# Kernel tuning notes

Measured on AMD Instinct MI355X. Metric: run time of the kernel, lower is better.

Reference implementation:

```python
import jax, jax.numpy as jnp
import numpy as np


def setup_inputs() -> dict:
    key = jax.random.key(0)
    ks = jax.random.split(key, 5)
    B, H, W, C, R = 4, 64, 64, 256, 32
    x = jax.random.normal(ks[0], (B, H, W, C), dtype=jnp.float32)
    # 1x1 conv kernels stored as [C_in, C_out] matrices (equivalent math)
    w_f = jax.random.normal(ks[1], (C, R), dtype=jnp.float32) * (1.0 / np.sqrt(C))
    w_g = jax.random.normal(ks[2], (C, R), dtype=jnp.float32) * (1.0 / np.sqrt(C))
    w_h = jax.random.normal(ks[3], (C, R), dtype=jnp.float32) * (1.0 / np.sqrt(C))
    w_v = jax.random.normal(ks[4], (R, C), dtype=jnp.float32) * (1.0 / np.sqrt(R))
    gamma = jnp.zeros((1,), dtype=jnp.float32)
    return {"x": x, "w_f": w_f, "w_g": w_g, "w_h": w_h, "w_v": w_v, "gamma": gamma}


def reference(x, w_f, w_g, w_h, w_v, gamma):
    B, H, W, C = x.shape
    N = H * W
    xt = x.reshape(B, N, C)                       # flatten spatial tokens
    f = jnp.einsum('bnc,cr->bnr', xt, w_f)        # 1x1 conv == token-wise matmul
    g = jnp.einsum('bnc,cr->bnr', xt, w_g)
    h = jnp.einsum('bnc,cr->bnr', xt, w_h)
    scores = jnp.einsum('bnr,bmr->bnm', f, g)     # [B, N, N]
    # NOTE: original softmaxes over axis=1 (the query/row axis), not axis=-1
    attn = jax.nn.softmax(scores, axis=1)
    y = jnp.einsum('bnm,bmr->bnr', attn, h)       # [B, N, R]
    y = jnp.einsum('bnr,rc->bnc', y, w_v)         # output 1x1 conv
    y = y.reshape(B, H, W, C)
    return gamma * y + x
```

## Files before the change

kernel.cpp:

```cpp
#include <hip/hip_runtime.h>


#define BB 4
#define NN 4096
#define CC 256
#define RR 32
#define CSEG 4
#define PSEG 4
#define MP 40
#define LOG2E 1.44269504088896340736f

typedef short short8 __attribute__((ext_vector_type(8)));
typedef float floatx4 __attribute__((ext_vector_type(4)));

#define MFMA16 __builtin_amdgcn_mfma_f32_16x16x32_bf16

static __device__ __forceinline__ unsigned short f2bf(float f) {
  union { float f; unsigned u; } v; v.f = f;
  const unsigned r = v.u + 0x7fffu + ((v.u >> 16) & 1u);
  return (unsigned short)(r >> 16);
}
static __device__ __forceinline__ unsigned bfpack(float lo, float hi) {
  return __builtin_amdgcn_perm(__float_as_uint(hi), __float_as_uint(lo), 0x07060302u);
}

__global__ __launch_bounds__(256) void k_prep(
    const float* __restrict__ wf, const float* __restrict__ wg,
    const float* __restrict__ wh, const float* __restrict__ wv,
    unsigned short* __restrict__ wfrag, unsigned short* __restrict__ wvfrag) {
  const int idx = blockIdx.x * 256 + threadIdx.x;
  const int lane = (idx >> 3) & 63;
  const int j = idx & 7;
  const int col = lane & 15, q = lane >> 4;
  if (idx < 24576) {
    const int mat = idx >> 13;
    const int fid = (idx >> 9) & 15;
    const int kc = fid >> 1, nt = fid & 1;
    const float* w = (mat == 0) ? wf : ((mat == 1) ? wg : wh);
    wfrag[idx] = f2bf(w[(kc * 32 + q * 8 + j) * RR + nt * 16 + col]);
  } else {
    const int r = idx - 24576;
    const int t = (r >> 9) & 15;
    wvfrag[r] = f2bf(wv[(q * 8 + j) * CC + t * 16 + col]);
  }
}

__global__ __launch_bounds__(256) void k_fgh(
    const float* __restrict__ x, const unsigned short* __restrict__ wfrag,
    unsigned short* __restrict__ f16, unsigned short* __restrict__ g16,
    unsigned short* __restrict__ hT16) {
  const int tid = threadIdx.x, lane = tid & 63, wave = tid >> 6;
  const int col = lane & 15, q = lane >> 4;
  const int t0 = blockIdx.x * 64 + wave * 16;
  short8 af[8];
  const float* xr = x + (long)(t0 + col) * CC + q * 8;
#pragma unroll
  for (int kc = 0; kc < 8; ++kc) {
    float tmp[8];
    *(float4*)(tmp) = *(const float4*)(xr + kc * 32);
    *(float4*)(tmp + 4) = *(const float4*)(xr + kc * 32 + 4);
    short8 o;
#pragma unroll
    for (int j = 0; j < 8; ++j) o[j] = (short)f2bf(tmp[j]);
    af[kc] = o;
  }
  const floatx4 zero = {0.f, 0.f, 0.f, 0.f};
  floatx4 acc[3][2];
#pragma unroll
  for (int m = 0; m < 3; ++m) { acc[m][0] = zero; acc[m][1] = zero; }
  const short8* wfr = (const short8*)wfrag;
#pragma unroll
  for (int kc = 0; kc < 8; ++kc) {
#pragma unroll
    for (int mat = 0; mat < 3; ++mat) {
#pragma unroll
      for (int nt = 0; nt < 2; ++nt) {
        const short8 bf = wfr[(mat * 16 + kc * 2 + nt) * 64 + lane];
        acc[mat][nt] = MFMA16(af[kc], bf, acc[mat][nt], 0, 0, 0);
      }
    }
  }
  const int b = t0 >> 12;
#pragma unroll
  for (int nt = 0; nt < 2; ++nt) {
#pragma unroll
    for (int r = 0; r < 4; ++r) {
      const int tok = t0 + q * 4 + r;
      const int n = nt * 16 + col;
      f16[(long)tok * RR + n] = f2bf(acc[0][nt][r] * LOG2E);
      g16[(long)tok * RR + n] = f2bf(acc[1][nt][r]);
      hT16[((long)b * RR + n) * NN + (tok & (NN - 1))] = f2bf(acc[2][nt][r]);
    }
  }
}

__global__ __launch_bounds__(256) void k_colsum(
    const unsigned short* __restrict__ f16, const unsigned short* __restrict__ g16,
    float* __restrict__ psum) {
  const int tid = threadIdx.x, lane = tid & 63, wave = tid >> 6;
  const int col = lane & 15, q = lane >> 4;
  const int mblk = blockIdx.x & 31;
  const int b = (blockIdx.x >> 5) & 3;
  const int seg = blockIdx.x >> 7;
  const int m0 = mblk * 128 + wave * 32;
  const short8 bg1 = *(const short8*)(g16 + ((long)(b * NN + m0 + col)) * RR + q * 8);
  const short8 bg2 = *(const short8*)(g16 + ((long)(b * NN + m0 + 16 + col)) * RR + q * 8);
  const floatx4 zero = {0.f, 0.f, 0.f, 0.f};
  float s1 = 0.f, s2 = 0.f;
  const unsigned short* fb = f16 + ((long)b * NN + seg * (NN / CSEG)) * RR;
#pragma unroll 4
  for (int n = 0; n < NN / CSEG; n += 16) {
    const short8 af = *(const short8*)(fb + (long)(n + col) * RR + q * 8);
    const floatx4 d1 = MFMA16(af, bg1, zero, 0, 0, 0);
    const floatx4 d2 = MFMA16(af, bg2, zero, 0, 0, 0);
    s1 += __builtin_amdgcn_exp2f(d1[0]) + __builtin_amdgcn_exp2f(d1[1]) +
          __builtin_amdgcn_exp2f(d1[2]) + __builtin_amdgcn_exp2f(d1[3]);
    s2 += __builtin_amdgcn_exp2f(d2[0]) + __builtin_amdgcn_exp2f(d2[1]) +
          __builtin_amdgcn_exp2f(d2[2]) + __builtin_amdgcn_exp2f(d2[3]);
  }
  s1 += __shfl_xor(s1, 16); s1 += __shfl_xor(s1, 32);
  s2 += __shfl_xor(s2, 16); s2 += __shfl_xor(s2, 32);
  if (lane < 16) {
    psum[(long)seg * (BB * NN) + b * NN + m0 + lane] = s1;
    psum[(long)seg * (BB * NN) + b * NN + m0 + 16 + lane] = s2;
  }
}

#define C_ADDR(TN, TM) (((TN) + col) * MP + (TM) + q * 4)
__global__ __launch_bounds__(256) void k_pv(
    const unsigned short* __restrict__ f16, const unsigned short* __restrict__ g16,
    const unsigned short* __restrict__ hT16, const float* __restrict__ psum,
    float* __restrict__ py) {
  __shared__ unsigned short pt_all[4][32 * MP];
  __shared__ float cis[NN / PSEG];
  const int tid = threadIdx.x, lane = tid & 63, wave = tid >> 6;
  const int col = lane & 15, q = lane >> 4;
  const int nblk = blockIdx.x & 31;
  const int b = (blockIdx.x >> 5) & 3;
  const int mseg = blockIdx.x >> 7;
  const int n0 = nblk * 128 + wave * 32;
  const int mbase = mseg * (NN / PSEG);
  for (int i = tid; i < NN / PSEG; i += 256) {
    float s = 0.f;
#pragma unroll
    for (int sg = 0; sg < CSEG; ++sg) s += psum[(long)sg * (BB * NN) + b * NN + mbase + i];
    cis[i] = 1.0f / s;
  }
  __syncthreads();
  const short8 af1 = *(const short8*)(f16 + ((long)(b * NN + n0 + col)) * RR + q * 8);
  const short8 af2 = *(const short8*)(f16 + ((long)(b * NN + n0 + 16 + col)) * RR + q * 8);
  const floatx4 zero = {0.f, 0.f, 0.f, 0.f};
  floatx4 a11 = zero, a12 = zero, a21 = zero, a22 = zero;
  unsigned short* pt = &pt_all[wave][0];
  const unsigned short* gb = g16 + (long)b * NN * RR;
  const unsigned short* hb = hT16 + (long)b * RR * NN;
  for (int mi = 0; mi < NN / PSEG; mi += 32) {
    const int m0 = mbase + mi;
    const short8 bg1 = *(const short8*)(gb + (long)(m0 + col) * RR + q * 8);
    const short8 bg2 = *(const short8*)(gb + (long)(m0 + 16 + col) * RR + q * 8);
    const floatx4 d00 = MFMA16(bg1, af1, zero, 0, 0, 0);
    const floatx4 d01 = MFMA16(bg2, af1, zero, 0, 0, 0);
    const floatx4 d10 = MFMA16(bg1, af2, zero, 0, 0, 0);
    const floatx4 d11 = MFMA16(bg2, af2, zero, 0, 0, 0);
    const float4 cia = *(const float4*)(cis + mi + q * 4);
    const float4 cib = *(const float4*)(cis + mi + 16 + q * 4);
    {
      float w0, w1, w2, w3;
      w0 = __builtin_amdgcn_exp2f(d00[0]) * cia.x; w1 = __builtin_amdgcn_exp2f(d00[1]) * cia.y;
      w2 = __builtin_amdgcn_exp2f(d00[2]) * cia.z; w3 = __builtin_amdgcn_exp2f(d00[3]) * cia.w;
      *(uint2*)(pt + C_ADDR(0, 0)) = make_uint2(bfpack(w0, w1), bfpack(w2, w3));
      w0 = __builtin_amdgcn_exp2f(d01[0]) * cib.x; w1 = __builtin_amdgcn_exp2f(d01[1]) * cib.y;
      w2 = __builtin_amdgcn_exp2f(d01[2]) * cib.z; w3 = __builtin_amdgcn_exp2f(d01[3]) * cib.w;
      *(uint2*)(pt + C_ADDR(0, 16)) = make_uint2(bfpack(w0, w1), bfpack(w2, w3));
      w0 = __builtin_amdgcn_exp2f(d10[0]) * cia.x; w1 = __builtin_amdgcn_exp2f(d10[1]) * cia.y;
      w2 = __builtin_amdgcn_exp2f(d10[2]) * cia.z; w3 = __builtin_amdgcn_exp2f(d10[3]) * cia.w;
      *(uint2*)(pt + C_ADDR(16, 0)) = make_uint2(bfpack(w0, w1), bfpack(w2, w3));
      w0 = __builtin_amdgcn_exp2f(d11[0]) * cib.x; w1 = __builtin_amdgcn_exp2f(d11[1]) * cib.y;
      w2 = __builtin_amdgcn_exp2f(d11[2]) * cib.z; w3 = __builtin_amdgcn_exp2f(d11[3]) * cib.w;
      *(uint2*)(pt + C_ADDR(16, 16)) = make_uint2(bfpack(w0, w1), bfpack(w2, w3));
    }
    const short8 ap1 = *(const short8*)(pt + col * MP + q * 8);
    const short8 ap2 = *(const short8*)(pt + (col + 16) * MP + q * 8);
    const short8 bh1 = *(const short8*)(hb + (long)col * NN + m0 + q * 8);
    const short8 bh2 = *(const short8*)(hb + (long)(col + 16) * NN + m0 + q * 8);
    a11 = MFMA16(ap1, bh1, a11, 0, 0, 0);
    a12 = MFMA16(ap1, bh2, a12, 0, 0, 0);
    a21 = MFMA16(ap2, bh1, a21, 0, 0, 0);
    a22 = MFMA16(ap2, bh2, a22, 0, 0, 0);
  }
  float* yp = py + (long)(mseg * BB + b) * NN * RR;
#pragma unroll
  for (int r = 0; r < 4; ++r) {
    yp[(long)(n0 + q * 4 + r) * RR + col]           = a11[r];
    yp[(long)(n0 + q * 4 + r) * RR + col + 16]      = a12[r];
    yp[(long)(n0 + 16 + q * 4 + r) * RR + col]      = a21[r];
    yp[(long)(n0 + 16 + q * 4 + r) * RR + col + 16] = a22[r];
  }
}

__global__ __launch_bounds__(256) void k_out(
    const float* __restrict__ py, const unsigned short* __restrict__ wvfrag,
    const float* __restrict__ x, const float* __restrict__ gamma,
    float* __restrict__ out) {
  __shared__ float ot[4][16 * 132];
  const int tid = threadIdx.x, lane = tid & 63, wave = tid >> 6;
  const int col = lane & 15, q = lane >> 4;
  const int t0 = blockIdx.x * 64 + wave * 16;
  const int b = t0 >> 12;
  const int tloc = t0 & (NN - 1);
  float s[8] = {0.f, 0.f, 0.f, 0.f, 0.f, 0.f, 0.f, 0.f};
#pragma unroll
  for (int sg = 0; sg < PSEG; ++sg) {
    const float* p = py + ((long)(sg * BB + b) * NN + tloc + col) * RR + q * 8;
    const float4 u0 = *(const float4*)p;
    const float4 u1 = *(const float4*)(p + 4);
    s[0] += u0.x; s[1] += u0.y; s[2] += u0.z; s[3] += u0.w;
    s[4] += u1.x; s[5] += u1.y; s[6] += u1.z; s[7] += u1.w;
  }
  short8 ay;
#pragma unroll
  for (int j = 0; j < 8; ++j) ay[j] = (short)f2bf(s[j]);
  const float gm = gamma[0];
  const floatx4 zero = {0.f, 0.f, 0.f, 0.f};
  const short8* wvf = (const short8*)wvfrag;
  float* pw = &ot[wave][0];
  const int tok = lane >> 2, cg = (lane & 3) * 4;
#pragma unroll
  for (int h = 0; h < 2; ++h) {
#pragma unroll
    for (int t = 0; t < 8; ++t) {
      const short8 bw = wvf[(h * 8 + t) * 64 + lane];
      const floatx4 d = MFMA16(ay, bw, zero, 0, 0, 0);
#pragma unroll
      for (int r = 0; r < 4; ++r) pw[(q * 4 + r) * 132 + t * 16 + col] = d[r];
    }
#pragma unroll
    for (int j = 0; j < 8; ++j) {
      const float4 v = *(const float4*)(pw + tok * 132 + cg + j * 16);
      const long gidx = (long)(t0 + tok) * CC + h * 128 + cg + j * 16;
      const float4 xv = *(const float4*)(x + gidx);
      float4 o;
      o.x = gm * v.x + xv.x; o.y = gm * v.y + xv.y;
      o.z = gm * v.z + xv.z; o.w = gm * v.w + xv.w;
      *(float4*)(out + gidx) = o;
    }
  }
}

extern "C" void kernel_launch(void* const* d_in, const int* in_sizes, int n_in,
                              void* d_out, int out_size, void* d_ws, size_t ws_size,
                              hipStream_t stream) {
  const float* x = (const float*)d_in[0];
  const float* wf = (const float*)d_in[1];
  const float* wg = (const float*)d_in[2];
  const float* wh = (const float*)d_in[3];
  const float* wv = (const float*)d_in[4];
  const float* gamma = (const float*)d_in[5];
  float* out = (float*)d_out;

  unsigned short* wfrag = (unsigned short*)d_ws;
  unsigned short* wvfrag = wfrag + 24576;
  unsigned short* f16 = wvfrag + 8192;
  unsigned short* g16 = f16 + (long)BB * NN * RR;
  unsigned short* hT16 = g16 + (long)BB * NN * RR;
  float* psum = (float*)(hT16 + (long)BB * NN * RR);
  float* py = psum + (long)CSEG * BB * NN;

  k_prep<<<128, 256, 0, stream>>>(wf, wg, wh, wv, wfrag, wvfrag);
  k_fgh<<<BB * NN / 64, 256, 0, stream>>>(x, wfrag, f16, g16, hT16);
  k_colsum<<<CSEG * BB * 32, 256, 0, stream>>>(f16, g16, psum);
  k_pv<<<PSEG * BB * 32, 256, 0, stream>>>(f16, g16, hT16, psum, py);
  k_out<<<BB * NN / 64, 256, 0, stream>>>(py, wvfrag, x, gamma, out);
}
```

Before: 131.7 us.

## Fuse five stage kernels into one cooperative kernel with grid syncs

Replaces the five separate launches (weight prep, f/g/h projection, column sums, PV, output projection) with a single cooperative kernel of 512 blocks that uses grid-wide barriers between stages. The aim is to remove per-launch overhead and inter-kernel gaps. The fgh and output stages now run on only two of four waves per block, with 32 tokens per block, and shared memory is aliased between stages. The cost is four grid barriers and a grid size limited by co-residency (launch bounds of 2 blocks per CU).

```diff
diff --git a/kernel.cpp b/kernel.cpp
--- a/kernel.cpp
+++ b/kernel.cpp
@@ -1,4 +1,7 @@
 #include <hip/hip_runtime.h>
+#include <hip/hip_cooperative_groups.h>
+
+namespace cg = cooperative_groups;
 
 
 #define BB 4
@@ -24,147 +27,143 @@
   return __builtin_amdgcn_perm(__float_as_uint(hi), __float_as_uint(lo), 0x07060302u);
 }
 
-__global__ __launch_bounds__(256) void k_prep(
-    const float* __restrict__ wf, const float* __restrict__ wg,
-    const float* __restrict__ wh, const float* __restrict__ wv,
-    unsigned short* __restrict__ wfrag, unsigned short* __restrict__ wvfrag) {
-  const int idx = blockIdx.x * 256 + threadIdx.x;
-  const int lane = (idx >> 3) & 63;
-  const int j = idx & 7;
-  const int col = lane & 15, q = lane >> 4;
-  if (idx < 24576) {
-    const int mat = idx >> 13;
-    const int fid = (idx >> 9) & 15;
-    const int kc = fid >> 1, nt = fid & 1;
-    const float* w = (mat == 0) ? wf : ((mat == 1) ? wg : wh);
-    wfrag[idx] = f2bf(w[(kc * 32 + q * 8 + j) * RR + nt * 16 + col]);
-  } else {
-    const int r = idx - 24576;
-    const int t = (r >> 9) & 15;
-    wvfrag[r] = f2bf(wv[(q * 8 + j) * CC + t * 16 + col]);
-  }
-}
-
-__global__ __launch_bounds__(256) void k_fgh(
-    const float* __restrict__ x, const unsigned short* __restrict__ wfrag,
+#define C_ADDR(TN, TM) (((TN) + col) * MP + (TM) + q * 4)
+
+__global__ __launch_bounds__(256, 2) void k_all(
+    const float* __restrict__ x, const float* __restrict__ wf,
+    const float* __restrict__ wg, const float* __restrict__ wh,
+    const float* __restrict__ wv, const float* __restrict__ gamma,
+    float* __restrict__ out,
+    unsigned short* __restrict__ wfrag, unsigned short* __restrict__ wvfrag,
     unsigned short* __restrict__ f16, unsigned short* __restrict__ g16,
-    unsigned short* __restrict__ hT16) {
+    unsigned short* __restrict__ hT16, float* __restrict__ psum,
+    float* __restrict__ py) {
+  cg::grid_group gg = cg::this_grid();
+  __shared__ __align__(16) unsigned char smem[16896];
   const int tid = threadIdx.x, lane = tid & 63, wave = tid >> 6;
   const int col = lane & 15, q = lane >> 4;
-  const int t0 = blockIdx.x * 64 + wave * 16;
-  short8 af[8];
-  const float* xr = x + (long)(t0 + col) * CC + q * 8;
-#pragma unroll
-  for (int kc = 0; kc < 8; ++kc) {
-    float tmp[8];
-    *(float4*)(tmp) = *(const float4*)(xr + kc * 32);
-    *(float4*)(tmp + 4) = *(const float4*)(xr + kc * 32 + 4);
-    short8 o;
-#pragma unroll
-    for (int j = 0; j < 8; ++j) o[j] = (short)f2bf(tmp[j]);
-    af[kc] = o;
-  }
+  const int blk = blockIdx.x;
   const floatx4 zero = {0.f, 0.f, 0.f, 0.f};
-  floatx4 acc[3][2];
-#pragma unroll
-  for (int m = 0; m < 3; ++m) { acc[m][0] = zero; acc[m][1] = zero; }
-  const short8* wfr = (const short8*)wfrag;
-#pragma unroll
-  for (int kc = 0; kc < 8; ++kc) {
-#pragma unroll
-    for (int mat = 0; mat < 3; ++mat) {
-#pragma unroll
-      for (int nt = 0; nt < 2; ++nt) {
-        const short8 bf = wfr[(mat * 16 + kc * 2 + nt) * 64 + lane];
-        acc[mat][nt] = MFMA16(af[kc], bf, acc[mat][nt], 0, 0, 0);
-      }
-    }
-  }
-  const int b = t0 >> 12;
-#pragma unroll
-  for (int nt = 0; nt < 2; ++nt) {
-#pragma unroll
-    for (int r = 0; r < 4; ++r) {
-      const int tok = t0 + q * 4 + r;
-      const int n = nt * 16 + col;
-      f16[(long)tok * RR + n] = f2bf(acc[0][nt][r] * LOG2E);
-      g16[(long)tok * RR + n] = f2bf(acc[1][nt][r]);
-      hT16[((long)b * RR + n) * NN + (tok & (NN - 1))] = f2bf(acc[2][nt][r]);
-    }
-  }
-}
-
-__global__ __launch_bounds__(256) void k_colsum(
-    const unsigned short* __restrict__ f16, const unsigned short* __restrict__ g16,
-    float* __restrict__ psum) {
-  const int tid = threadIdx.x, lane = tid & 63, wave = tid >> 6;
-  const int col = lane & 15, q = lane >> 4;
-  const int mblk = blockIdx.x & 31;
-  const int b = (blockIdx.x >> 5) & 3;
-  const int seg = blockIdx.x >> 7;
-  const int m0 = mblk * 128 + wave * 32;
-  const short8 bg1 = *(const short8*)(g16 + ((long)(b * NN + m0 + col)) * RR + q * 8);
-  const short8 bg2 = *(const short8*)(g16 + ((long)(b * NN + m0 + 16 + col)) * RR + q * 8);
-  const floatx4 zero = {0.f, 0.f, 0.f, 0.f};
-  float s1 = 0.f, s2 = 0.f;
-  const unsigned short* fb = f16 + ((long)b * NN + seg * (NN / CSEG)) * RR;
+
+  {
+    const int idx = blk * 256 + tid;
+    if (idx < 24576) {
+      const int mat = idx >> 13;
+      const int fid = (idx >> 9) & 15;
+      const int kc = fid >> 1, nt = fid & 1;
+      const int l2 = (idx >> 3) & 63, j = idx & 7;
+      const int c2 = l2 & 15, q2 = l2 >> 4;
+      const float* w = (mat == 0) ? wf : ((mat == 1) ? wg : wh);
+      wfrag[idx] = f2bf(w[(kc * 32 + q2 * 8 + j) * RR + nt * 16 + c2]);
+    } else if (idx < 32768) {
+      const int r = idx - 24576;
+      const int t = (r >> 9) & 15;
+      const int l2 = (r >> 3) & 63, j = r & 7;
+      const int c2 = l2 & 15, q2 = l2 >> 4;
+      wvfrag[r] = f2bf(wv[(q2 * 8 + j) * CC + t * 16 + c2]);
+    }
+  }
+  gg.sync();
+
+  if (wave < 2) {
+    const int t0 = blk * 32 + wave * 16;
+    short8 af[8];
+    const float* xr = x + (long)(t0 + col) * CC + q * 8;
+#pragma unroll
+    for (int kc = 0; kc < 8; ++kc) {
+      float tmp[8];
+      *(float4*)(tmp) = *(const float4*)(xr + kc * 32);
+      *(float4*)(tmp + 4) = *(const float4*)(xr + kc * 32 + 4);
+      short8 o;
+#pragma unroll
+      for (int j = 0; j < 8; ++j) o[j] = (short)f2bf(tmp[j]);
+      af[kc] = o;
+    }
+    floatx4 acc[3][2];
+#pragma unroll
+    for (int m = 0; m < 3; ++m) { acc[m][0] = zero; acc[m][1] = zero; }
+    const short8* wfr = (const short8*)wfrag;
+#pragma unroll
+    for (int kc = 0; kc < 8; ++kc) {
+#pragma unroll
+      for (int mat = 0; mat < 3; ++mat) {
+#pragma unroll
+        for (int nt = 0; nt < 2; ++nt) {
+          const short8 bf = wfr[(mat * 16 + kc * 2 + nt) * 64 + lane];
+          acc[mat][nt] = MFMA16(af[kc], bf, acc[mat][nt], 0, 0, 0);
+        }
+      }
+    }
+    const int b = t0 >> 12;
+#pragma unroll
+    for (int nt = 0; nt < 2; ++nt) {
+#pragma unroll
+      for (int r = 0; r < 4; ++r) {
+        const int tok = t0 + q * 4 + r;
+        const int n = nt * 16 + col;
+        f16[(long)tok * RR + n] = f2bf(acc[0][nt][r] * LOG2E);
+        g16[(long)tok * RR + n] = f2bf(acc[1][nt][r]);
+        hT16[((long)b * RR + n) * NN + (tok & (NN - 1))] = f2bf(acc[2][nt][r]);
+      }
+    }
+  }
+  gg.sync();
+
+  {
+    const int mblk = blk & 31, b = (blk >> 5) & 3, seg = blk >> 7;
+    const int m0 = mblk * 128 + wave * 32;
+    const short8 bg1 = *(const short8*)(g16 + ((long)(b * NN + m0 + col)) * RR + q * 8);
+    const short8 bg2 = *(const short8*)(g16 + ((long)(b * NN + m0 + 16 + col)) * RR + q * 8);
+    float s1 = 0.f, s2 = 0.f;
+    const unsigned short* fb = f16 + ((long)b * NN + seg * (NN / CSEG)) * RR;
 #pragma unroll 4
-  for (int n = 0; n < NN / CSEG; n += 16) {
-    const short8 af = *(const short8*)(fb + (long)(n + col) * RR + q * 8);
-    const floatx4 d1 = MFMA16(af, bg1, zero, 0, 0, 0);
-    const floatx4 d2 = MFMA16(af, bg2, zero, 0, 0, 0);
-    s1 += __builtin_amdgcn_exp2f(d1[0]) + __builtin_amdgcn_exp2f(d1[1]) +
-          __builtin_amdgcn_exp2f(d1[2]) + __builtin_amdgcn_exp2f(d1[3]);
-    s2 += __builtin_amdgcn_exp2f(d2[0]) + __builtin_amdgcn_exp2f(d2[1]) +
-          __builtin_amdgcn_exp2f(d2[2]) + __builtin_amdgcn_exp2f(d2[3]);
-  }
-  s1 += __shfl_xor(s1, 16); s1 += __shfl_xor(s1, 32);
-  s2 += __shfl_xor(s2, 16); s2 += __shfl_xor(s2, 32);
-  if (lane < 16) {
-    psum[(long)seg * (BB * NN) + b * NN + m0 + lane] = s1;
-    psum[(long)seg * (BB * NN) + b * NN + m0 + 16 + lane] = s2;
-  }
-}
-
-#define C_ADDR(TN, TM) (((TN) + col) * MP + (TM) + q * 4)
-__global__ __launch_bounds__(256) void k_pv(
-    const unsigned short* __restrict__ f16, const unsigned short* __restrict__ g16,
-    const unsigned short* __restrict__ hT16, const float* __restrict__ psum,
-    float* __restrict__ py) {
-  __shared__ unsigned short pt_all[4][32 * MP];
-  __shared__ float cis[NN / PSEG];
-  const int tid = threadIdx.x, lane = tid & 63, wave = tid >> 6;
-  const int col = lane & 15, q = lane >> 4;
-  const int nblk = blockIdx.x & 31;
-  const int b = (blockIdx.x >> 5) & 3;
-  const int mseg = blockIdx.x >> 7;
-  const int n0 = nblk * 128 + wave * 32;
-  const int mbase = mseg * (NN / PSEG);
-  for (int i = tid; i < NN / PSEG; i += 256) {
-    float s = 0.f;
-#pragma unroll
-    for (int sg = 0; sg < CSEG; ++sg) s += psum[(long)sg * (BB * NN) + b * NN + mbase + i];
-    cis[i] = 1.0f / s;
-  }
-  __syncthreads();
-  const short8 af1 = *(const short8*)(f16 + ((long)(b * NN + n0 + col)) * RR + q * 8);
-  const short8 af2 = *(const short8*)(f16 + ((long)(b * NN + n0 + 16 + col)) * RR + q * 8);
-  const floatx4 zero = {0.f, 0.f, 0.f, 0.f};
-  floatx4 a11 = zero, a12 = zero, a21 = zero, a22 = zero;
-  unsigned short* pt = &pt_all[wave][0];
-  const unsigned short* gb = g16 + (long)b * NN * RR;
-  const unsigned short* hb = hT16 + (long)b * RR * NN;
-  for (int mi = 0; mi < NN / PSEG; mi += 32) {
-    const int m0 = mbase + mi;
-    const short8 bg1 = *(const short8*)(gb + (long)(m0 + col) * RR + q * 8);
-    const short8 bg2 = *(const short8*)(gb + (long)(m0 + 16 + col) * RR + q * 8);
-    const floatx4 d00 = MFMA16(bg1, af1, zero, 0, 0, 0);
-    const floatx4 d01 = MFMA16(bg2, af1, zero, 0, 0, 0);
-    const floatx4 d10 = MFMA16(bg1, af2, zero, 0, 0, 0);
-    const floatx4 d11 = MFMA16(bg2, af2, zero, 0, 0, 0);
-    const float4 cia = *(const float4*)(cis + mi + q * 4);
-    const float4 cib = *(const float4*)(cis + mi + 16 + q * 4);
-    {
+    for (int n = 0; n < NN / CSEG; n += 16) {
+      const short8 af = *(const short8*)(fb + (long)(n + col) * RR + q * 8);
+      const floatx4 d1 = MFMA16(af, bg1, zero, 0, 0, 0);
+      const floatx4 d2 = MFMA16(af, bg2, zero, 0, 0, 0);
+      s1 += __builtin_amdgcn_exp2f(d1[0]) + __builtin_amdgcn_exp2f(d1[1]) +
+            __builtin_amdgcn_exp2f(d1[2]) + __builtin_amdgcn_exp2f(d1[3]);
+      s2 += __builtin_amdgcn_exp2f(d2[0]) + __builtin_amdgcn_exp2f(d2[1]) +
+            __builtin_amdgcn_exp2f(d2[2]) + __builtin_amdgcn_exp2f(d2[3]);
+    }
+    s1 += __shfl_xor(s1, 16); s1 += __shfl_xor(s1, 32);
+    s2 += __shfl_xor(s2, 16); s2 += __shfl_xor(s2, 32);
+    if (lane < 16) {
+      psum[(long)seg * (BB * NN) + b * NN + m0 + lane] = s1;
+      psum[(long)seg * (BB * NN) + b * NN + m0 + 16 + lane] = s2;
+    }
+  }
+  gg.sync();
+
+  {
+    unsigned short* pt = (unsigned short*)smem + wave * (32 * MP);
+    float* cis = (float*)(smem + 4 * 32 * MP * 2);
+    const int nblk = blk & 31, b = (blk >> 5) & 3, mseg = blk >> 7;
+    const int n0 = nblk * 128 + wave * 32;
+    const int mbase = mseg * (NN / PSEG);
+    for (int i = tid; i < NN / PSEG; i += 256) {
+      float s = 0.f;
+#pragma unroll
+      for (int sg = 0; sg < CSEG; ++sg)
+        s += psum[(long)sg * (BB * NN) + b * NN + mbase + i];
+      cis[i] = 1.0f / s;
+    }
+    __syncthreads();
+    const short8 af1 = *(const short8*)(f16 + ((long)(b * NN + n0 + col)) * RR + q * 8);
+    const short8 af2 = *(const short8*)(f16 + ((long)(b * NN + n0 + 16 + col)) * RR + q * 8);
+    floatx4 a11 = zero, a12 = zero, a21 = zero, a22 = zero;
+    const unsigned short* gb = g16 + (long)b * NN * RR;
+    const unsigned short* hb = hT16 + (long)b * RR * NN;
+    for (int mi = 0; mi < NN / PSEG; mi += 32) {
+      const int m0 = mbase + mi;
+      const short8 bg1 = *(const short8*)(gb + (long)(m0 + col) * RR + q * 8);
+      const short8 bg2 = *(const short8*)(gb + (long)(m0 + 16 + col) * RR + q * 8);
+      const floatx4 d00 = MFMA16(bg1, af1, zero, 0, 0, 0);
+      const floatx4 d01 = MFMA16(bg2, af1, zero, 0, 0, 0);
+      const floatx4 d10 = MFMA16(bg1, af2, zero, 0, 0, 0);
+      const floatx4 d11 = MFMA16(bg2, af2, zero, 0, 0, 0);
+      const float4 cia = *(const float4*)(cis + mi + q * 4);
+      const float4 cib = *(const float4*)(cis + mi + 16 + q * 4);
       float w0, w1, w2, w3;
       w0 = __builtin_amdgcn_exp2f(d00[0]) * cia.x; w1 = __builtin_amdgcn_exp2f(d00[1]) * cia.y;
       w2 = __builtin_amdgcn_exp2f(d00[2]) * cia.z; w3 = __builtin_amdgcn_exp2f(d00[3]) * cia.w;
@@ -178,71 +177,65 @@
       w0 = __builtin_amdgcn_exp2f(d11[0]) * cib.x; w1 = __builtin_amdgcn_exp2f(d11[1]) * cib.y;
       w2 = __builtin_amdgcn_exp2f(d11[2]) * cib.z; w3 = __builtin_amdgcn_exp2f(d11[3]) * cib.w;
       *(uint2*)(pt + C_ADDR(16, 16)) = make_uint2(bfpack(w0, w1), bfpack(w2, w3));
-    }
-    const short8 ap1 = *(const short8*)(pt + col * MP + q * 8);
-    const short8 ap2 = *(const short8*)(pt + (col + 16) * MP + q * 8);
-    const short8 bh1 = *(const short8*)(hb + (long)col * NN + m0 + q * 8);
-    const short8 bh2 = *(const short8*)(hb + (long)(col + 16) * NN + m0 + q * 8);
-    a11 = MFMA16(ap1, bh1, a11, 0, 0, 0);
-    a12 = MFMA16(ap1, bh2, a12, 0, 0, 0);
-    a21 = MFMA16(ap2, bh1, a21, 0, 0, 0);
-    a22 = MFMA16(ap2, bh2, a22, 0, 0, 0);
-  }
-  float* yp = py + (long)(mseg * BB + b) * NN * RR;
-#pragma unroll
-  for (int r = 0; r < 4; ++r) {
-    yp[(long)(n0 + q * 4 + r) * RR + col]           = a11[r];
-    yp[(long)(n0 + q * 4 + r) * RR + col + 16]      = a12[r];
-    yp[(long)(n0 + 16 + q * 4 + r) * RR + col]      = a21[r];
-    yp[(long)(n0 + 16 + q * 4 + r) * RR + col + 16] = a22[r];
-  }
-}
-
-__global__ __launch_bounds__(256) void k_out(
-    const float* __restrict__ py, const unsigned short* __restrict__ wvfrag,
-    const float* __restrict__ x, const float* __restrict__ gamma,
-    float* __restrict__ out) {
-  __shared__ float ot[4][16 * 132];
-  const int tid = threadIdx.x, lane = tid & 63, wave = tid >> 6;
-  const int col = lane & 15, q = lane >> 4;
-  const int t0 = blockIdx.x * 64 + wave * 16;
-  const int b = t0 >> 12;
-  const int tloc = t0 & (NN - 1);
-  float s[8] = {0.f, 0.f, 0.f, 0.f, 0.f, 0.f, 0.f, 0.f};
-#pragma unroll
-  for (int sg = 0; sg < PSEG; ++sg) {
-    const float* p = py + ((long)(sg * BB + b) * NN + tloc + col) * RR + q * 8;
-    const float4 u0 = *(const float4*)p;
-    const float4 u1 = *(const float4*)(p + 4);
-    s[0] += u0.x; s[1] += u0.y; s[2] += u0.z; s[3] += u0.w;
-    s[4] += u1.x; s[5] += u1.y; s[6] += u1.z; s[7] += u1.w;
-  }
-  short8 ay;
-#pragma unroll
-  for (int j = 0; j < 8; ++j) ay[j] = (short)f2bf(s[j]);
-  const float gm = gamma[0];
-  const floatx4 zero = {0.f, 0.f, 0.f, 0.f};
-  const short8* wvf = (const short8*)wvfrag;
-  float* pw = &ot[wave][0];
-  const int tok = lane >> 2, cg = (lane & 3) * 4;
-#pragma unroll
-  for (int h = 0; h < 2; ++h) {
-#pragma unroll
-    for (int t = 0; t < 8; ++t) {
-      const short8 bw = wvf[(h * 8 + t) * 64 + lane];
-      const floatx4 d = MFMA16(ay, bw, zero, 0, 0, 0);
-#pragma unroll
-      for (int r = 0; r < 4; ++r) pw[(q * 4 + r) * 132 + t * 16 + col] = d[r];
-    }
-#pragma unroll
-    for (int j = 0; j < 8; ++j) {
-      const float4 v = *(const float4*)(pw + tok * 132 + cg + j * 16);
-      const long gidx = (long)(t0 + tok) * CC + h * 128 + cg + j * 16;
-      const float4 xv = *(const float4*)(x + gidx);
-      float4 o;
-      o.x = gm * v.x + xv.x; o.y = gm * v.y + xv.y;
-      o.z = gm * v.z + xv.z; o.w = gm * v.w + xv.w;
-      *(float4*)(out + gidx) = o;
+      const short8 ap1 = *(const short8*)(pt + col * MP + q * 8);
+      const short8 ap2 = *(const short8*)(pt + (col + 16) * MP + q * 8);
+      const short8 bh1 = *(const short8*)(hb + (long)col * NN + m0 + q * 8);
+      const short8 bh2 = *(const short8*)(hb + (long)(col + 16) * NN + m0 + q * 8);
+      a11 = MFMA16(ap1, bh1, a11, 0, 0, 0);
+      a12 = MFMA16(ap1, bh2, a12, 0, 0, 0);
+      a21 = MFMA16(ap2, bh1, a21, 0, 0, 0);
+      a22 = MFMA16(ap2, bh2, a22, 0, 0, 0);
+    }
+    float* yp = py + (long)(mseg * BB + b) * NN * RR;
+#pragma unroll
+    for (int r = 0; r < 4; ++r) {
+      yp[(long)(n0 + q * 4 + r) * RR + col]           = a11[r];
+      yp[(long)(n0 + q * 4 + r) * RR + col + 16]      = a12[r];
+      yp[(long)(n0 + 16 + q * 4 + r) * RR + col]      = a21[r];
+      yp[(long)(n0 + 16 + q * 4 + r) * RR + col + 16] = a22[r];
+    }
+  }
+  gg.sync();
+
+  if (wave < 2) {
+    float* pw = (float*)smem + wave * (16 * 132);
+    const int t0 = blk * 32 + wave * 16;
+    const int b = t0 >> 12;
+    const int tloc = t0 & (NN - 1);
+    float s[8] = {0.f, 0.f, 0.f, 0.f, 0.f, 0.f, 0.f, 0.f};
+#pragma unroll
+    for (int sg = 0; sg < PSEG; ++sg) {
+      const float* p = py + ((long)(sg * BB + b) * NN + tloc + col) * RR + q * 8;
+      const float4 u0 = *(const float4*)p;
+      const float4 u1 = *(const float4*)(p + 4);
+      s[0] += u0.x; s[1] += u0.y; s[2] += u0.z; s[3] += u0.w;
+      s[4] += u1.x; s[5] += u1.y; s[6] += u1.z; s[7] += u1.w;
+    }
+    short8 ay;
+#pragma unroll
+    for (int j = 0; j < 8; ++j) ay[j] = (short)f2bf(s[j]);
+    const float gm = gamma[0];
+    const short8* wvf = (const short8*)wvfrag;
+    const int tok = lane >> 2, cg2 = (lane & 3) * 4;
+#pragma unroll
+    for (int h = 0; h < 2; ++h) {
+#pragma unroll
+      for (int t = 0; t < 8; ++t) {
+        const short8 bw = wvf[(h * 8 + t) * 64 + lane];
+        const floatx4 d = MFMA16(ay, bw, zero, 0, 0, 0);
+#pragma unroll
+        for (int r = 0; r < 4; ++r) pw[(q * 4 + r) * 132 + t * 16 + col] = d[r];
+      }
+#pragma unroll
+      for (int j = 0; j < 8; ++j) {
+        const float4 v = *(const float4*)(pw + tok * 132 + cg2 + j * 16);
+        const long gidx = (long)(t0 + tok) * CC + h * 128 + cg2 + j * 16;
+        const float4 xv = *(const float4*)(x + gidx);
+        float4 o;
+        o.x = gm * v.x + xv.x; o.y = gm * v.y + xv.y;
+        o.z = gm * v.z + xv.z; o.w = gm * v.w + xv.w;
+        *(float4*)(out + gidx) = o;
+      }
     }
   }
 }
@@ -266,9 +259,7 @@
   float* psum = (float*)(hT16 + (long)BB * NN * RR);
   float* py = psum + (long)CSEG * BB * NN;
 
-  k_prep<<<128, 256, 0, stream>>>(wf, wg, wh, wv, wfrag, wvfrag);
-  k_fgh<<<BB * NN / 64, 256, 0, stream>>>(x, wfrag, f16, g16, hT16);
-  k_colsum<<<CSEG * BB * 32, 256, 0, stream>>>(f16, g16, psum);
-  k_pv<<<PSEG * BB * 32, 256, 0, stream>>>(f16, g16, hT16, psum, py);
-  k_out<<<BB * NN / 64, 256, 0, stream>>>(py, wvfrag, x, gamma, out);
-}
+  void* args[] = {&x, &wf, &wg, &wh, &wv, &gamma, &out,
+                  &wfrag, &wvfrag, &f16, &g16, &hT16, &psum, &py};
+  hipLaunchCooperativeKernel((void*)k_all, dim3(512), dim3(256), args, 0, stream);
+}
```

Measured after the change: 345.6 us. 162% more time.

## Fuse PV and output projection, fold weight prep into LDS staging

Applied to the files above, without the earlier changes.

Removes the separate weight-prep kernel: each k_fgh and k_pvout block now converts the fp32 weights to bf16 MFMA fragments in shared memory. The PV and output-projection kernels are merged into one kernel. Each block handles 32 query tokens, splits the key range in half across wave pairs, and reduces the two partial results in LDS, so the fp32 partial-y buffer is no longer written to and read back from global memory. In exchange, every block redoes the weight conversion and the full column-sum reciprocal, only half the waves take part in the output stage, and the per-wave PV tile shrinks from 32 to 16 queries, which reduces reuse of the g and h loads.

```diff
diff --git a/kernel.cpp b/kernel.cpp
--- a/kernel.cpp
+++ b/kernel.cpp
@@ -6,7 +6,6 @@
 #define CC 256
 #define RR 32
 #define CSEG 4
-#define PSEG 4
 #define MP 40
 #define LOG2E 1.44269504088896340736f
 
@@ -24,33 +23,30 @@
   return __builtin_amdgcn_perm(__float_as_uint(hi), __float_as_uint(lo), 0x07060302u);
 }
 
-__global__ __launch_bounds__(256) void k_prep(
-    const float* __restrict__ wf, const float* __restrict__ wg,
-    const float* __restrict__ wh, const float* __restrict__ wv,
-    unsigned short* __restrict__ wfrag, unsigned short* __restrict__ wvfrag) {
-  const int idx = blockIdx.x * 256 + threadIdx.x;
-  const int lane = (idx >> 3) & 63;
-  const int j = idx & 7;
-  const int col = lane & 15, q = lane >> 4;
-  if (idx < 24576) {
-    const int mat = idx >> 13;
-    const int fid = (idx >> 9) & 15;
-    const int kc = fid >> 1, nt = fid & 1;
-    const float* w = (mat == 0) ? wf : ((mat == 1) ? wg : wh);
-    wfrag[idx] = f2bf(w[(kc * 32 + q * 8 + j) * RR + nt * 16 + col]);
-  } else {
-    const int r = idx - 24576;
-    const int t = (r >> 9) & 15;
-    wvfrag[r] = f2bf(wv[(q * 8 + j) * CC + t * 16 + col]);
-  }
-}
-
 __global__ __launch_bounds__(256) void k_fgh(
-    const float* __restrict__ x, const unsigned short* __restrict__ wfrag,
+    const float* __restrict__ x, const float* __restrict__ wf,
+    const float* __restrict__ wg, const float* __restrict__ wh,
     unsigned short* __restrict__ f16, unsigned short* __restrict__ g16,
     unsigned short* __restrict__ hT16) {
+  __shared__ unsigned short wflds[24576];
   const int tid = threadIdx.x, lane = tid & 63, wave = tid >> 6;
   const int col = lane & 15, q = lane >> 4;
+  for (int s4 = tid; s4 < 6144; s4 += 256) {
+    const int mat = s4 >> 11;
+    const int s = (s4 & 2047) << 2;
+    const int rr = s >> 5, c = s & 31;
+    const float* w = (mat == 0) ? wf : ((mat == 1) ? wg : wh);
+    const float4 v = *(const float4*)(w + s);
+    const int kc = rr >> 5, q2 = (rr >> 3) & 3, j = rr & 7;
+    const int base = (mat * 16 + kc * 2) * 512 + q2 * 128 + j;
+    const float vv[4] = {v.x, v.y, v.z, v.w};
+#pragma unroll
+    for (int e = 0; e < 4; ++e) {
+      const int ce = c + e;
+      wflds[base + (ce >> 4) * 512 + (ce & 15) * 8] = f2bf(vv[e]);
+    }
+  }
+  __syncthreads();
   const int t0 = blockIdx.x * 64 + wave * 16;
   short8 af[8];
   const float* xr = x + (long)(t0 + col) * CC + q * 8;
@@ -68,14 +64,13 @@
   floatx4 acc[3][2];
 #pragma unroll
   for (int m = 0; m < 3; ++m) { acc[m][0] = zero; acc[m][1] = zero; }
-  const short8* wfr = (const short8*)wfrag;
 #pragma unroll
   for (int kc = 0; kc < 8; ++kc) {
 #pragma unroll
     for (int mat = 0; mat < 3; ++mat) {
 #pragma unroll
       for (int nt = 0; nt < 2; ++nt) {
-        const short8 bf = wfr[(mat * 16 + kc * 2 + nt) * 64 + lane];
+        const short8 bf = *(const short8*)(wflds + (mat * 16 + kc * 2 + nt) * 512 + lane * 8);
         acc[mat][nt] = MFMA16(af[kc], bf, acc[mat][nt], 0, 0, 0);
       }
     }
@@ -126,123 +121,114 @@
   }
 }
 
-#define C_ADDR(TN, TM) (((TN) + col) * MP + (TM) + q * 4)
-__global__ __launch_bounds__(256) void k_pv(
+__global__ __launch_bounds__(256, 2) void k_pvout(
     const unsigned short* __restrict__ f16, const unsigned short* __restrict__ g16,
     const unsigned short* __restrict__ hT16, const float* __restrict__ psum,
-    float* __restrict__ py) {
-  __shared__ unsigned short pt_all[4][32 * MP];
-  __shared__ float cis[NN / PSEG];
+    const float* __restrict__ wv, const float* __restrict__ x,
+    const float* __restrict__ gamma, float* __restrict__ out) {
+  __shared__ unsigned short wvlds[8192];
+  __shared__ float cis[NN];
+  __shared__ unsigned short pt_all[4][16 * MP];
+  __shared__ float ylds[4][16 * 36];
+  __shared__ float ot[2][16 * 132];
   const int tid = threadIdx.x, lane = tid & 63, wave = tid >> 6;
   const int col = lane & 15, q = lane >> 4;
-  const int nblk = blockIdx.x & 31;
-  const int b = (blockIdx.x >> 5) & 3;
-  const int mseg = blockIdx.x >> 7;
-  const int n0 = nblk * 128 + wave * 32;
-  const int mbase = mseg * (NN / PSEG);
-  for (int i = tid; i < NN / PSEG; i += 256) {
+  const int b = blockIdx.x >> 7;
+  const int t0 = (blockIdx.x & 127) * 32 + (wave & 1) * 16;
+  const int half = wave >> 1;
+  for (int s4 = tid; s4 < 2048; s4 += 256) {
+    const int s = s4 << 2;
+    const int rr = s >> 8, c = s & 255;
+    const float4 v = *(const float4*)(wv + s);
+    const int base = (rr >> 3) * 128 + (rr & 7);
+    const float vv[4] = {v.x, v.y, v.z, v.w};
+#pragma unroll
+    for (int e = 0; e < 4; ++e) {
+      const int ce = c + e;
+      wvlds[(ce >> 4) * 512 + base + (ce & 15) * 8] = f2bf(vv[e]);
+    }
+  }
+  for (int i = tid; i < NN; i += 256) {
     float s = 0.f;
 #pragma unroll
-    for (int sg = 0; sg < CSEG; ++sg) s += psum[(long)sg * (BB * NN) + b * NN + mbase + i];
+    for (int sg = 0; sg < CSEG; ++sg) s += psum[(long)sg * (BB * NN) + b * NN + i];
     cis[i] = 1.0f / s;
   }
   __syncthreads();
-  const short8 af1 = *(const short8*)(f16 + ((long)(b * NN + n0 + col)) * RR + q * 8);
-  const short8 af2 = *(const short8*)(f16 + ((long)(b * NN + n0 + 16 + col)) * RR + q * 8);
   const floatx4 zero = {0.f, 0.f, 0.f, 0.f};
-  floatx4 a11 = zero, a12 = zero, a21 = zero, a22 = zero;
+  const short8 bf = *(const short8*)(f16 + ((long)(b * NN + t0 + col)) * RR + q * 8);
+  floatx4 acc1 = zero, acc2 = zero;
   unsigned short* pt = &pt_all[wave][0];
   const unsigned short* gb = g16 + (long)b * NN * RR;
   const unsigned short* hb = hT16 + (long)b * RR * NN;
-  for (int mi = 0; mi < NN / PSEG; mi += 32) {
-    const int m0 = mbase + mi;
-    const short8 bg1 = *(const short8*)(gb + (long)(m0 + col) * RR + q * 8);
-    const short8 bg2 = *(const short8*)(gb + (long)(m0 + 16 + col) * RR + q * 8);
-    const floatx4 d00 = MFMA16(bg1, af1, zero, 0, 0, 0);
-    const floatx4 d01 = MFMA16(bg2, af1, zero, 0, 0, 0);
-    const floatx4 d10 = MFMA16(bg1, af2, zero, 0, 0, 0);
-    const floatx4 d11 = MFMA16(bg2, af2, zero, 0, 0, 0);
+  const int m_end = half * 2048 + 2048;
+#pragma unroll 2
+  for (int mi = half * 2048; mi < m_end; mi += 32) {
+    const short8 bg1 = *(const short8*)(gb + (long)(mi + col) * RR + q * 8);
+    const short8 bg2 = *(const short8*)(gb + (long)(mi + 16 + col) * RR + q * 8);
+    const floatx4 d0 = MFMA16(bg1, bf, zero, 0, 0, 0);
+    const floatx4 d1 = MFMA16(bg2, bf, zero, 0, 0, 0);
     const float4 cia = *(const float4*)(cis + mi + q * 4);
     const float4 cib = *(const float4*)(cis + mi + 16 + q * 4);
+    float w0, w1, w2, w3;
+    w0 = __builtin_amdgcn_exp2f(d0[0]) * cia.x; w1 = __builtin_amdgcn_exp2f(d0[1]) * cia.y;
+    w2 = __builtin_amdgcn_exp2f(d0[2]) * cia.z; w3 = __builtin_amdgcn_exp2f(d0[3]) * cia.w;
+    *(uint2*)(pt + col * MP + q * 4) = make_uint2(bfpack(w0, w1), bfpack(w2, w3));
+    w0 = __builtin_amdgcn_exp2f(d1[0]) * cib.x; w1 = __builtin_amdgcn_exp2f(d1[1]) * cib.y;
+    w2 = __builtin_amdgcn_exp2f(d1[2]) * cib.z; w3 = __builtin_amdgcn_exp2f(d1[3]) * cib.w;
+    *(uint2*)(pt + col * MP + 16 + q * 4) = make_uint2(bfpack(w0, w1), bfpack(w2, w3));
+    const short8 ap = *(const short8*)(pt + col * MP + q * 8);
+    const short8 bh1 = *(const short8*)(hb + (long)col * NN + mi + q * 8);
+    const short8 bh2 = *(const short8*)(hb + (long)(col + 16) * NN + mi + q * 8);
+    acc1 = MFMA16(ap, bh1, acc1, 0, 0, 0);
+    acc2 = MFMA16(ap, bh2, acc2, 0, 0, 0);
+  }
+  {
+    float* yp = &ylds[(wave & 1) * 2 + half][0];
+#pragma unroll
+    for (int r = 0; r < 4; ++r) {
+      yp[(q * 4 + r) * 36 + col] = acc1[r];
+      yp[(q * 4 + r) * 36 + col + 16] = acc2[r];
+    }
+  }
+  __syncthreads();
+  if (wave < 2) {
+    const float* y0 = &ylds[wave * 2][0];
+    const float* y1 = &ylds[wave * 2 + 1][0];
+    float s[8];
     {
-      float w0, w1, w2, w3;
-      w0 = __builtin_amdgcn_exp2f(d00[0]) * cia.x; w1 = __builtin_amdgcn_exp2f(d00[1]) * cia.y;
-      w2 = __builtin_amdgcn_exp2f(d00[2]) * cia.z; w3 = __builtin_amdgcn_exp2f(d00[3]) * cia.w;
-      *(uint2*)(pt + C_ADDR(0, 0)) = make_uint2(bfpack(w0, w1), bfpack(w2, w3));
-      w0 = __builtin_amdgcn_exp2f(d01[0]) * cib.x; w1 = __builtin_amdgcn_exp2f(d01[1]) * cib.y;
-      w2 = __builtin_amdgcn_exp2f(d01[2]) * cib.z; w3 = __builtin_amdgcn_exp2f(d01[3]) * cib.w;
-      *(uint2*)(pt + C_ADDR(0, 16)) = make_uint2(bfpack(w0, w1), bfpack(w2, w3));
-      w0 = __builtin_amdgcn_exp2f(d10[0]) * cia.x; w1 = __builtin_amdgcn_exp2f(d10[1]) * cia.y;
-      w2 = __builtin_amdgcn_exp2f(d10[2]) * cia.z; w3 = __builtin_amdgcn_exp2f(d10[3]) * cia.w;
-      *(uint2*)(pt + C_ADDR(16, 0)) = make_uint2(bfpack(w0, w1), bfpack(w2, w3));
-      w0 = __builtin_amdgcn_exp2f(d11[0]) * cib.x; w1 = __builtin_amdgcn_exp2f(d11[1]) * cib.y;
-      w2 = __builtin_amdgcn_exp2f(d11[2]) * cib.z; w3 = __builtin_amdgcn_exp2f(d11[3]) * cib.w;
-      *(uint2*)(pt + C_ADDR(16, 16)) = make_uint2(bfpack(w0, w1), bfpack(w2, w3));
-    }
-    const short8 ap1 = *(const short8*)(pt + col * MP + q * 8);
-    const short8 ap2 = *(const short8*)(pt + (col + 16) * MP + q * 8);
-    const short8 bh1 = *(const short8*)(hb + (long)col * NN + m0 + q * 8);
-    const short8 bh2 = *(const short8*)(hb + (long)(col + 16) * NN + m0 + q * 8);
-    a11 = MFMA16(ap1, bh1, a11, 0, 0, 0);
-    a12 = MFMA16(ap1, bh2, a12, 0, 0, 0);
-    a21 = MFMA16(ap2, bh1, a21, 0, 0, 0);
-    a22 = MFMA16(ap2, bh2, a22, 0, 0, 0);
-  }
-  float* yp = py + (long)(mseg * BB + b) * NN * RR;
-#pragma unroll
-  for (int r = 0; r < 4; ++r) {
-    yp[(long)(n0 + q * 4 + r) * RR + col]           = a11[r];
-    yp[(long)(n0 + q * 4 + r) * RR + col + 16]      = a12[r];
-    yp[(long)(n0 + 16 + q * 4 + r) * RR + col]      = a21[r];
-    yp[(long)(n0 + 16 + q * 4 + r) * RR + col + 16] = a22[r];
-  }
-}
-
-__global__ __launch_bounds__(256) void k_out(
-    const float* __restrict__ py, const unsigned short* __restrict__ wvfrag,
-    const float* __restrict__ x, const float* __restrict__ gamma,
-    float* __restrict__ out) {
-  __shared__ float ot[4][16 * 132];
-  const int tid = threadIdx.x, lane = tid & 63, wave = tid >> 6;
-  const int col = lane & 15, q = lane >> 4;
-  const int t0 = blockIdx.x * 64 + wave * 16;
-  const int b = t0 >> 12;
-  const int tloc = t0 & (NN - 1);
-  float s[8] = {0.f, 0.f, 0.f, 0.f, 0.f, 0.f, 0.f, 0.f};
-#pragma unroll
-  for (int sg = 0; sg < PSEG; ++sg) {
-    const float* p = py + ((long)(sg * BB + b) * NN + tloc + col) * RR + q * 8;
-    const float4 u0 = *(const float4*)p;
-    const float4 u1 = *(const float4*)(p + 4);
-    s[0] += u0.x; s[1] += u0.y; s[2] += u0.z; s[3] += u0.w;
-    s[4] += u1.x; s[5] += u1.y; s[6] += u1.z; s[7] += u1.w;
-  }
-  short8 ay;
-#pragma unroll
-  for (int j = 0; j < 8; ++j) ay[j] = (short)f2bf(s[j]);
-  const float gm = gamma[0];
-  const floatx4 zero = {0.f, 0.f, 0.f, 0.f};
-  const short8* wvf = (const short8*)wvfrag;
-  float* pw = &ot[wave][0];
-  const int tok = lane >> 2, cg = (lane & 3) * 4;
-#pragma unroll
-  for (int h = 0; h < 2; ++h) {
-#pragma unroll
-    for (int t = 0; t < 8; ++t) {
-      const short8 bw = wvf[(h * 8 + t) * 64 + lane];
-      const floatx4 d = MFMA16(ay, bw, zero, 0, 0, 0);
-#pragma unroll
-      for (int r = 0; r < 4; ++r) pw[(q * 4 + r) * 132 + t * 16 + col] = d[r];
-    }
-#pragma unroll
-    for (int j = 0; j < 8; ++j) {
-      const float4 v = *(const float4*)(pw + tok * 132 + cg + j * 16);
-      const long gidx = (long)(t0 + tok) * CC + h * 128 + cg + j * 16;
-      const float4 xv = *(const float4*)(x + gidx);
-      float4 o;
-      o.x = gm * v.x + xv.x; o.y = gm * v.y + xv.y;
-      o.z = gm * v.z + xv.z; o.w = gm * v.w + xv.w;
-      *(float4*)(out + gidx) = o;
+      const float4 a0 = *(const float4*)(y0 + col * 36 + q * 8);
+      const float4 a1 = *(const float4*)(y0 + col * 36 + q * 8 + 4);
+      const float4 b0 = *(const float4*)(y1 + col * 36 + q * 8);
+      const float4 b1 = *(const float4*)(y1 + col * 36 + q * 8 + 4);
+      s[0] = a0.x + b0.x; s[1] = a0.y + b0.y; s[2] = a0.z + b0.z; s[3] = a0.w + b0.w;
+      s[4] = a1.x + b1.x; s[5] = a1.y + b1.y; s[6] = a1.z + b1.z; s[7] = a1.w + b1.w;
+    }
+    short8 ay;
+#pragma unroll
+    for (int j = 0; j < 8; ++j) ay[j] = (short)f2bf(s[j]);
+    const float gm = gamma[0];
+    float* pw = &ot[wave][0];
+    const int tok = lane >> 2, cg2 = (lane & 3) * 4;
+#pragma unroll
+    for (int hh = 0; hh < 2; ++hh) {
+#pragma unroll
+      for (int t = 0; t < 8; ++t) {
+        const short8 bw = *(const short8*)(wvlds + (hh * 8 + t) * 512 + lane * 8);
+        const floatx4 d = MFMA16(ay, bw, zero, 0, 0, 0);
+#pragma unroll
+        for (int r = 0; r < 4; ++r) pw[(q * 4 + r) * 132 + t * 16 + col] = d[r];
+      }
+#pragma unroll
+      for (int j = 0; j < 8; ++j) {
+        const float4 v = *(const float4*)(pw + tok * 132 + cg2 + j * 16);
+        const long gidx = (long)(b * NN + t0 + tok) * CC + hh * 128 + cg2 + j * 16;
+        const float4 xv = *(const float4*)(x + gidx);
+        float4 o;
+        o.x = gm * v.x + xv.x; o.y = gm * v.y + xv.y;
+        o.z = gm * v.z + xv.z; o.w = gm * v.w + xv.w;
+        *(float4*)(out + gidx) = o;
+      }
     }
   }
 }
@@ -258,17 +244,12 @@
   const float* gamma = (const float*)d_in[5];
   float* out = (float*)d_out;
 
-  unsigned short* wfrag = (unsigned short*)d_ws;
-  unsigned short* wvfrag = wfrag + 24576;
-  unsigned short* f16 = wvfrag + 8192;
+  unsigned short* f16 = (unsigned short*)d_ws;
   unsigned short* g16 = f16 + (long)BB * NN * RR;
   unsigned short* hT16 = g16 + (long)BB * NN * RR;
   float* psum = (float*)(hT16 + (long)BB * NN * RR);
-  float* py = psum + (long)CSEG * BB * NN;
-
-  k_prep<<<128, 256, 0, stream>>>(wf, wg, wh, wv, wfrag, wvfrag);
-  k_fgh<<<BB * NN / 64, 256, 0, stream>>>(x, wfrag, f16, g16, hT16);
+
+  k_fgh<<<BB * NN / 64, 256, 0, stream>>>(x, wf, wg, wh, f16, g16, hT16);
   k_colsum<<<CSEG * BB * 32, 256, 0, stream>>>(f16, g16, psum);
-  k_pv<<<PSEG * BB * 32, 256, 0, stream>>>(f16, g16, hT16, psum, py);
-  k_out<<<BB * NN / 64, 256, 0, stream>>>(py, wvfrag, x, gamma, out);
-}
+  k_pvout<<<BB * 128, 256, 0, stream>>>(f16, g16, hT16, psum, wv, x, gamma, out);
+}
```

After: 153.0 us. 16.1% more time.
